# Performance work log

Hardware: AMD Instinct MI355X
Metric: run time of the kernel (lower is better)

The kernel has to match this reference:

```python
import jax, jax.numpy as jnp
import numpy as np

N = 10000      # nodes
E = 160000     # edges
F_IN = 128     # input_feature
G = 64         # graphs in batch
NC = 10        # num_classes
H1, H2, H3 = 1000, 700, 200


def _xavier(k, fi, fo):
    lim = float(np.sqrt(6.0 / (fi + fo)))
    return jax.random.uniform(k, (fi, fo), jnp.float32, -lim, lim)


def setup_inputs() -> dict:
    key = jax.random.key(0)
    ks = jax.random.split(key, 8)
    x = jax.random.normal(ks[0], (N, F_IN), jnp.float32)
    edge_index = jax.random.randint(ks[1], (2, E), 0, N)
    batch = jnp.sort(jax.random.randint(ks[2], (N,), 0, G))
    return {
        "x": x,
        "edge_index": edge_index,
        "batch": batch,
        "W1": _xavier(ks[3], F_IN, H1), "b1": jnp.zeros((H1,), jnp.float32),
        "W2": _xavier(ks[4], H1, H2),   "b2": jnp.zeros((H2,), jnp.float32),
        "W3": _xavier(ks[5], H2, H3),   "b3": jnp.zeros((H3,), jnp.float32),
        "Wl": _xavier(ks[6], H3, NC),   "bl": jnp.zeros((NC,), jnp.float32),
    }


def _gcn_conv(x, W, b, src, dst, dinv):
    # GCNConv: h = xW; out_i = sum_{j->i} d_j^-1/2 d_i^-1/2 h_j + d_i^-1 h_i + b
    h = x @ W
    coef = dinv[src] * dinv[dst]                      # [E]
    agg = jax.ops.segment_sum(h[src] * coef[:, None], dst, num_segments=N)
    agg = agg + h * (dinv * dinv)[:, None]            # self-loop term
    return agg + b


def reference(x, edge_index, batch, W1, b1, W2, b2, W3, b3, Wl, bl):
    src, dst = edge_index[0], edge_index[1]
    # degree with self-loops (edge weight 1), computed on target nodes
    deg = jax.ops.segment_sum(jnp.ones((E,), x.dtype), dst, num_segments=N) + 1.0
    dinv = jax.lax.rsqrt(deg)

    h = jax.nn.relu(_gcn_conv(x, W1, b1, src, dst, dinv))
    h = jax.nn.relu(_gcn_conv(h, W2, b2, src, dst, dinv))
    h = jax.nn.relu(_gcn_conv(h, W3, b3, src, dst, dinv))

    # global_mean_pool over graph ids
    s = jax.ops.segment_sum(h, batch, num_segments=G)
    cnt = jax.ops.segment_sum(jnp.ones((N,), h.dtype), batch, num_segments=G)
    pooled = s / jnp.maximum(cnt, 1.0)[:, None]

    # dropout is identity in eval mode
    return pooled @ Wl + bl
```

## Files before the change

### kernel.cpp

```cpp
#include <hip/hip_runtime.h>
#include <hip/hip_bf16.h>
#include <stdint.h>


#define SLOT 64

__device__ __forceinline__ uint16_t f2b(float f) {
    union { float f; uint32_t u; } v; v.f = f;
    return (uint16_t)((v.u + 0x7fffu + ((v.u >> 16) & 1u)) >> 16);
}
__device__ __forceinline__ float blo(uint32_t u) { union { uint32_t u; float f; } v; v.u = u << 16; return v.f; }
__device__ __forceinline__ float bhi(uint32_t u) { union { uint32_t u; float f; } v; v.u = u & 0xffff0000u; return v.f; }

__global__ __launch_bounds__(256) void k_scatter(
    const int* __restrict__ src, const int* __restrict__ dst,
    int* __restrict__ cursor, int* __restrict__ slots, int E, int N) {
    int g  = blockIdx.x & 7;
    int nb = gridDim.x >> 3;
    int b  = blockIdx.x >> 3;
    int seg = (N + 7) >> 3;
    int lo = g * seg;
    int hi = lo + seg; if (hi > N) hi = N;
    int per = (E + nb - 1) / nb;
    int e0 = b * per;
    int e1 = e0 + per; if (e1 > E) e1 = E;
    for (int e = e0 + threadIdx.x; e < e1; e += 256) {
        int d = dst[e];
        if (d >= lo && d < hi) {
            int s = src[e];
            int pos = atomicAdd(&cursor[d], 1);
            if (pos < SLOT) slots[d * SLOT + pos] = s;
        }
    }
}

__global__ void k_prep(const float* __restrict__ W1, const float* __restrict__ W2,
                       const float* __restrict__ W3,
                       uint16_t* __restrict__ T1, uint16_t* __restrict__ T2,
                       uint16_t* __restrict__ T3,
                       const float* __restrict__ b1, const float* __restrict__ b2,
                       const float* __restrict__ b3,
                       float* __restrict__ p1, float* __restrict__ p2,
                       float* __restrict__ p3,
                       const float* __restrict__ x, uint16_t* __restrict__ xb,
                       const int* __restrict__ deg, float* __restrict__ dinv,
                       int N, int F, int H1, int H2, int H3,
                       int Fp, int H1p, int H2p, int H3p, int n8) {
    __shared__ float tile[32][33];
    int z = blockIdx.z;
    if (z < 3) {
        const float* W; uint16_t* T; int K, Nn, Kp, Np;
        if (z == 0)      { W = W1; T = T1; K = F;  Nn = H1; Kp = Fp;  Np = H1p; }
        else if (z == 1) { W = W2; T = T2; K = H1; Nn = H2; Kp = H1p; Np = H2p; }
        else             { W = W3; T = T3; K = H2; Nn = H3; Kp = H2p; Np = H3p; }
        if ((int)blockIdx.x * 32 >= Kp || (int)blockIdx.y * 32 >= Np) return;
        int k0 = blockIdx.x * 32, n0 = blockIdx.y * 32;
        int tx = threadIdx.x, ty = threadIdx.y;
        for (int i = ty; i < 32; i += 8) {
            int k = k0 + i, n = n0 + tx;
            tile[i][tx] = (k < K && n < Nn) ? W[(size_t)k * Nn + n] : 0.f;
        }
        __syncthreads();
        for (int i = ty; i < 32; i += 8) {
            int n = n0 + i, k = k0 + tx;
            T[(size_t)n * Kp + k] = f2b(tile[tx][i]);
        }
    } else {
        int id = (blockIdx.y * gridDim.x + blockIdx.x) * 256 + threadIdx.y * 32 + threadIdx.x;
        if (z == 3) {
            if (id < H1p) p1[id] = (id < H1) ? b1[id] : 0.f;
            else if (id < H1p + H2p) { int k = id - H1p; p2[k] = (k < H2) ? b2[k] : 0.f; }
            else if (id < H1p + H2p + H3p) { int k = id - H1p - H2p; p3[k] = (k < H3) ? b3[k] : 0.f; }
        } else if (z == 4) {
            if (id < n8) {
                int node = id / (F >> 3);
                float dv = rsqrtf((float)deg[node] + 1.0f);
                const float4* x4 = (const float4*)x;
                float4 a = x4[2 * id], b = x4[2 * id + 1];
                uint4 o;
                o.x = (uint32_t)f2b(a.x * dv) | ((uint32_t)f2b(a.y * dv) << 16);
                o.y = (uint32_t)f2b(a.z * dv) | ((uint32_t)f2b(a.w * dv) << 16);
                o.z = (uint32_t)f2b(b.x * dv) | ((uint32_t)f2b(b.y * dv) << 16);
                o.w = (uint32_t)f2b(b.z * dv) | ((uint32_t)f2b(b.w * dv) << 16);
                ((uint4*)xb)[id] = o;
            }
        } else {
            if (id < N) dinv[id] = rsqrtf((float)deg[id] + 1.0f);
        }
    }
}

__global__ __launch_bounds__(256) void k_agg_panel(
    const uint16_t* __restrict__ in, uint16_t* __restrict__ out,
    const int* __restrict__ deg_, const int* __restrict__ slots,
    const float* __restrict__ dinv, const float* __restrict__ bias,
    int N, int Hc, int pc, int P, int relu) {
    int slotg = blockIdx.x & 7;
    int panel = slotg % P;
    int seg   = slotg / P;
    int nseg  = 8 / P;
    int segLen = (N + nseg - 1) / nseg;
    int wave = threadIdx.x >> 6, lane = threadIdx.x & 63;
    int half = lane >> 5, sub = lane & 31;
    int item = (blockIdx.x >> 3) * 128 + wave * 32 + sub;
    int rel = item / pc;
    if (rel >= segLen) return;
    int node = seg * segLen + rel;
    if (node >= N) return;
    int j = panel * pc + (item - rel * pc);
    int deg = deg_[node];
    if (deg > SLOT) deg = SLOT;
    int base = node * SLOT;
    float dv = dinv[node];
    const uint4* in4 = (const uint4*)in;
    float a[8] = {0.f, 0.f, 0.f, 0.f, 0.f, 0.f, 0.f, 0.f};
    if (half == 0) {
        uint4 v = in4[(size_t)node * Hc + j];
        a[0] = blo(v.x); a[1] = bhi(v.x);
        a[2] = blo(v.y); a[3] = bhi(v.y);
        a[4] = blo(v.z); a[5] = bhi(v.z);
        a[6] = blo(v.w); a[7] = bhi(v.w);
    }
    int D8 = deg & ~7;
    int e = 4 * half;
    if (e < D8) {
        int4 q = *(const int4*)&slots[base + e];
        uint4 h0 = in4[(size_t)q.x * Hc + j];
        uint4 h1 = in4[(size_t)q.y * Hc + j];
        uint4 h2 = in4[(size_t)q.z * Hc + j];
        uint4 h3 = in4[(size_t)q.w * Hc + j];
        for (e += 8; e < D8; e += 8) {
            int4 qn = *(const int4*)&slots[base + e];
            uint4 g0 = in4[(size_t)qn.x * Hc + j];
            uint4 g1 = in4[(size_t)qn.y * Hc + j];
            uint4 g2 = in4[(size_t)qn.z * Hc + j];
            uint4 g3 = in4[(size_t)qn.w * Hc + j];
            a[0] += blo(h0.x); a[1] += bhi(h0.x);
            a[2] += blo(h0.y); a[3] += bhi(h0.y);
            a[4] += blo(h0.z); a[5] += bhi(h0.z);
            a[6] += blo(h0.w); a[7] += bhi(h0.w);
            a[0] += blo(h1.x); a[1] += bhi(h1.x);
            a[2] += blo(h1.y); a[3] += bhi(h1.y);
            a[4] += blo(h1.z); a[5] += bhi(h1.z);
            a[6] += blo(h1.w); a[7] += bhi(h1.w);
            a[0] += blo(h2.x); a[1] += bhi(h2.x);
            a[2] += blo(h2.y); a[3] += bhi(h2.y);
            a[4] += blo(h2.z); a[5] += bhi(h2.z);
            a[6] += blo(h2.w); a[7] += bhi(h2.w);
            a[0] += blo(h3.x); a[1] += bhi(h3.x);
            a[2] += blo(h3.y); a[3] += bhi(h3.y);
            a[4] += blo(h3.z); a[5] += bhi(h3.z);
            a[6] += blo(h3.w); a[7] += bhi(h3.w);
            h0 = g0; h1 = g1; h2 = g2; h3 = g3;
        }
        a[0] += blo(h0.x); a[1] += bhi(h0.x);
        a[2] += blo(h0.y); a[3] += bhi(h0.y);
        a[4] += blo(h0.z); a[5] += bhi(h0.z);
        a[6] += blo(h0.w); a[7] += bhi(h0.w);
        a[0] += blo(h1.x); a[1] += bhi(h1.x);
        a[2] += blo(h1.y); a[3] += bhi(h1.y);
        a[4] += blo(h1.z); a[5] += bhi(h1.z);
        a[6] += blo(h1.w); a[7] += bhi(h1.w);
        a[0] += blo(h2.x); a[1] += bhi(h2.x);
        a[2] += blo(h2.y); a[3] += bhi(h2.y);
        a[4] += blo(h2.z); a[5] += bhi(h2.z);
        a[6] += blo(h2.w); a[7] += bhi(h2.w);
        a[0] += blo(h3.x); a[1] += bhi(h3.x);
        a[2] += blo(h3.y); a[3] += bhi(h3.y);
        a[4] += blo(h3.z); a[5] += bhi(h3.z);
        a[6] += blo(h3.w); a[7] += bhi(h3.w);
    }
    int t0 = half ? (D8 + 4 < deg ? D8 + 4 : deg) : D8;
    int t1 = half ? deg : (D8 + 4 < deg ? D8 + 4 : deg);
    for (int ee = t0; ee < t1; ++ee) {
        int s0 = slots[base + ee];
        uint4 h = in4[(size_t)s0 * Hc + j];
        a[0] += blo(h.x); a[1] += bhi(h.x);
        a[2] += blo(h.y); a[3] += bhi(h.y);
        a[4] += blo(h.z); a[5] += bhi(h.z);
        a[6] += blo(h.w); a[7] += bhi(h.w);
    }
#pragma unroll
    for (int t = 0; t < 8; ++t) a[t] += __shfl_xor(a[t], 32, 64);
    if (half == 0) {
        if (bias) {
            const float4* b4 = (const float4*)bias;
            float4 b0 = b4[2 * j], b1 = b4[2 * j + 1];
            a[0] = fmaf(a[0], dv, b0.x); a[1] = fmaf(a[1], dv, b0.y);
            a[2] = fmaf(a[2], dv, b0.z); a[3] = fmaf(a[3], dv, b0.w);
            a[4] = fmaf(a[4], dv, b1.x); a[5] = fmaf(a[5], dv, b1.y);
            a[6] = fmaf(a[6], dv, b1.z); a[7] = fmaf(a[7], dv, b1.w);
        } else {
#pragma unroll
            for (int t = 0; t < 8; ++t) a[t] *= dv;
        }
        if (relu) {
#pragma unroll
            for (int t = 0; t < 8; ++t) a[t] = fmaxf(a[t], 0.f);
        }
        uint4 o;
        o.x = (uint32_t)f2b(a[0]) | ((uint32_t)f2b(a[1]) << 16);
        o.y = (uint32_t)f2b(a[2]) | ((uint32_t)f2b(a[3]) << 16);
        o.z = (uint32_t)f2b(a[4]) | ((uint32_t)f2b(a[5]) << 16);
        o.w = (uint32_t)f2b(a[6]) | ((uint32_t)f2b(a[7]) << 16);
        ((uint4*)out)[(size_t)node * Hc + j] = o;
    }
}

__global__ __launch_bounds__(256) void k_pool_cls(
    const uint16_t* __restrict__ h, const int* __restrict__ batch,
    const float* __restrict__ Wl, const float* __restrict__ bl,
    float* __restrict__ out, int N, int H, int Hc, int NC) {
    __shared__ float part[8][26][8];
    __shared__ float pooled[200];
    int g = blockIdx.x;
    int tid = threadIdx.x;
    int lo = 0, hi = N;
    while (lo < hi) { int m = (lo + hi) >> 1; if (batch[m] < g) lo = m + 1; else hi = m; }
    int start = lo; hi = N;
    while (lo < hi) { int m = (lo + hi) >> 1; if (batch[m] < g + 1) lo = m + 1; else hi = m; }
    int end = lo;
    int j = tid & 31, s = tid >> 5;
    int jmax = H >> 3;
    const uint4* h4 = (const uint4*)h;
    if (j < jmax) {
        float a[8] = {0.f, 0.f, 0.f, 0.f, 0.f, 0.f, 0.f, 0.f};
        for (int node = start + s; node < end; node += 8) {
            uint4 v = h4[(size_t)node * Hc + j];
            a[0] += blo(v.x); a[1] += bhi(v.x);
            a[2] += blo(v.y); a[3] += bhi(v.y);
            a[4] += blo(v.z); a[5] += bhi(v.z);
            a[6] += blo(v.w); a[7] += bhi(v.w);
        }
#pragma unroll
        for (int t = 0; t < 8; ++t) part[s][j][t] = a[t];
    }
    __syncthreads();
    if (tid < H) {
        float sum = 0.f;
#pragma unroll
        for (int ss = 0; ss < 8; ++ss) sum += part[ss][tid >> 3][tid & 7];
        pooled[tid] = sum;
    }
    __syncthreads();
    if (tid < 64) {
        float scale = 1.0f / fmaxf((float)(end - start), 1.0f);
        int c = tid & 15, q = tid >> 4;
        float acc = 0.f;
        if (c < NC) {
            for (int k = q; k < H; k += 4)
                acc += pooled[k] * Wl[(size_t)k * NC + c];
        }
        acc += __shfl_xor(acc, 16, 64);
        acc += __shfl_xor(acc, 32, 64);
        if (q == 0 && c < NC) out[(size_t)g * NC + c] = acc * scale + bl[c];
    }
}

typedef __attribute__((ext_vector_type(8))) short short8;
typedef __attribute__((ext_vector_type(4))) float floatx4;

#define LDSP(p) ((__attribute__((address_space(3))) void*)(uintptr_t)(p))
#define GLBP(p) ((const __attribute__((address_space(1))) void*)(uintptr_t)(p))

__global__ __launch_bounds__(256) void k_gemm128(
    const uint16_t* __restrict__ A, const uint16_t* __restrict__ Bt,
    const float* __restrict__ bias, uint16_t* __restrict__ Cout,
    int M, int Kp, int Np, int relu, int nrg, int nr,
    const float* __restrict__ rowscale) {
    int bid = blockIdx.x;
    int rsub = bid & 7;
    int t_ = bid >> 3;
    int rg = t_ % nrg, cc = t_ / nrg;
    int rt = rg * 8 + rsub;
    if (rt >= nr) return;
    int row0 = rt * 128, col0 = cc * 128;

    __shared__ uint16_t As[128 * 64];
    __shared__ uint16_t Bs[128 * 64];
    int tid = threadIdx.x;
    int wave = tid >> 6, lane = tid & 63;
    int quad = lane >> 4, m16 = lane & 15;
    int wr = wave >> 1, wc = wave & 1;

    int rA = tid >> 3;
    int cA = (tid & 7) ^ (rA & 7);
    const uint16_t* gA = A  + (size_t)(row0 + rA) * Kp + cA * 8;
    const uint16_t* gB = Bt + (size_t)(col0 + rA) * Kp + cA * 8;
    uint16_t* lA = As + tid * 8;
    uint16_t* lB = Bs + tid * 8;
    size_t rowStep32 = (size_t)32 * Kp;

    floatx4 acc[4][4];
#pragma unroll
    for (int i = 0; i < 4; ++i)
#pragma unroll
        for (int j = 0; j < 4; ++j) acc[i][j] = (floatx4){0.f, 0.f, 0.f, 0.f};

    const short* Ash = (const short*)As;
    const short* Bsh = (const short*)Bs;
    int swA = m16 & 7;

    for (int k0 = 0; k0 < Kp; k0 += 64) {
#pragma unroll
        for (int p = 0; p < 4; ++p) {
            __builtin_amdgcn_global_load_lds(GLBP(gA + p * rowStep32), LDSP(lA + p * 2048), 16, 0, 0);
            __builtin_amdgcn_global_load_lds(GLBP(gB + p * rowStep32), LDSP(lB + p * 2048), 16, 0, 0);
        }
        gA += 64; gB += 64;
        __syncthreads();
#pragma unroll
        for (int h = 0; h < 2; ++h) {
            short8 af[4], bf[4];
            int c = h * 4 + quad;
            int pos = (c ^ swA) * 8;
#pragma unroll
            for (int i = 0; i < 4; ++i)
                af[i] = *(const short8*)&Ash[(wr * 64 + i * 16 + m16) * 64 + pos];
#pragma unroll
            for (int j = 0; j < 4; ++j)
                bf[j] = *(const short8*)&Bsh[(wc * 64 + j * 16 + m16) * 64 + pos];
#pragma unroll
            for (int i = 0; i < 4; ++i)
#pragma unroll
                for (int j = 0; j < 4; ++j)
                    acc[i][j] = __builtin_amdgcn_mfma_f32_16x16x32_bf16(af[i], bf[j], acc[i][j], 0, 0, 0);
        }
        __syncthreads();
    }

    float bv[4];
#pragma unroll
    for (int j = 0; j < 4; ++j) {
        int n = col0 + wc * 64 + j * 16 + m16;
        bv[j] = bias ? bias[n] : 0.f;
    }
#pragma unroll
    for (int i = 0; i < 4; ++i) {
        int mBase = row0 + wr * 64 + i * 16 + quad * 4;
#pragma unroll
        for (int r = 0; r < 4; ++r) {
            int m = mBase + r;
            if (m < M) {
                float s = rowscale ? rowscale[m] : 1.f;
#pragma unroll
                for (int j = 0; j < 4; ++j) {
                    int n = col0 + wc * 64 + j * 16 + m16;
                    float v = acc[i][j][r] * s + bv[j];
                    if (relu) v = fmaxf(v, 0.f);
                    Cout[(size_t)m * Np + n] = f2b(v);
                }
            }
        }
    }
}

__global__ __launch_bounds__(256) void k_gemm64(
    const uint16_t* __restrict__ A, const uint16_t* __restrict__ Bt,
    const float* __restrict__ bias, uint16_t* __restrict__ Cout,
    int M, int Kp, int Np, int relu, int nrg, int nr,
    const float* __restrict__ rowscale) {
    int bid = blockIdx.x;
    int rsub = bid & 7;
    int t_ = bid >> 3;
    int rg = t_ % nrg, cc = t_ / nrg;
    int rt = rg * 8 + rsub;
    if (rt >= nr) return;
    int row0 = rt * 128, col0 = cc * 64;

    __shared__ uint16_t As[128 * 64];
    __shared__ uint16_t Bs[64 * 64];
    int tid = threadIdx.x;
    int wave = tid >> 6, lane = tid & 63;
    int quad = lane >> 4, m16 = lane & 15;
    int wr = wave >> 1, wc = wave & 1;

    int rA = tid >> 3;
    int cA = (tid & 7) ^ (rA & 7);
    const uint16_t* gA = A  + (size_t)(row0 + rA) * Kp + cA * 8;
    const uint16_t* gB = Bt + (size_t)(col0 + rA) * Kp + cA * 8;
    uint16_t* lA = As + tid * 8;
    uint16_t* lB = Bs + tid * 8;
    size_t rowStep32 = (size_t)32 * Kp;

    floatx4 acc[4][2];
#pragma unroll
    for (int i = 0; i < 4; ++i)
#pragma unroll
        for (int j = 0; j < 2; ++j) acc[i][j] = (floatx4){0.f, 0.f, 0.f, 0.f};

    const short* Ash = (const short*)As;
    const short* Bsh = (const short*)Bs;
    int swA = m16 & 7;

    for (int k0 = 0; k0 < Kp; k0 += 64) {
#pragma unroll
        for (int p = 0; p < 4; ++p)
            __builtin_amdgcn_global_load_lds(GLBP(gA + p * rowStep32), LDSP(lA + p * 2048), 16, 0, 0);
#pragma unroll
        for (int p = 0; p < 2; ++p)
            __builtin_amdgcn_global_load_lds(GLBP(gB + p * rowStep32), LDSP(lB + p * 2048), 16, 0, 0);
        gA += 64; gB += 64;
        __syncthreads();
#pragma unroll
        for (int h = 0; h < 2; ++h) {
            short8 af[4], bf[2];
            int c = h * 4 + quad;
            int pos = (c ^ swA) * 8;
#pragma unroll
            for (int i = 0; i < 4; ++i)
                af[i] = *(const short8*)&Ash[(wr * 64 + i * 16 + m16) * 64 + pos];
#pragma unroll
            for (int j = 0; j < 2; ++j)
                bf[j] = *(const short8*)&Bsh[(wc * 32 + j * 16 + m16) * 64 + pos];
#pragma unroll
            for (int i = 0; i < 4; ++i)
#pragma unroll
                for (int j = 0; j < 2; ++j)
                    acc[i][j] = __builtin_amdgcn_mfma_f32_16x16x32_bf16(af[i], bf[j], acc[i][j], 0, 0, 0);
        }
        __syncthreads();
    }

    float bv[2];
#pragma unroll
    for (int j = 0; j < 2; ++j) {
        int n = col0 + wc * 32 + j * 16 + m16;
        bv[j] = bias ? bias[n] : 0.f;
    }
#pragma unroll
    for (int i = 0; i < 4; ++i) {
        int mBase = row0 + wr * 64 + i * 16 + quad * 4;
#pragma unroll
        for (int r = 0; r < 4; ++r) {
            int m = mBase + r;
            if (m < M) {
                float s = rowscale ? rowscale[m] : 1.f;
#pragma unroll
                for (int j = 0; j < 2; ++j) {
                    int n = col0 + wc * 32 + j * 16 + m16;
                    float v = acc[i][j][r] * s + bv[j];
                    if (relu) v = fmaxf(v, 0.f);
                    Cout[(size_t)m * Np + n] = f2b(v);
                }
            }
        }
    }
}

static inline size_t align256(size_t x) { return (x + 255) & ~(size_t)255; }
static inline int pad128(int x) { return (x + 127) & ~127; }

extern "C" void kernel_launch(void* const* d_in, const int* in_sizes, int n_in,
                              void* d_out, int out_size, void* d_ws, size_t ws_size,
                              hipStream_t stream) {
    const float* x   = (const float*)d_in[0];
    const int*   ei  = (const int*)d_in[1];
    const int*   bat = (const int*)d_in[2];
    const float* W1  = (const float*)d_in[3];
    const float* b1  = (const float*)d_in[4];
    const float* W2  = (const float*)d_in[5];
    const float* b2  = (const float*)d_in[6];
    const float* W3  = (const float*)d_in[7];
    const float* b3  = (const float*)d_in[8];
    const float* Wl  = (const float*)d_in[9];
    const float* bl  = (const float*)d_in[10];

    const int N  = in_sizes[2];
    const int E  = in_sizes[1] / 2;
    const int F  = in_sizes[0] / N;
    const int H1 = in_sizes[4];
    const int H2 = in_sizes[6];
    const int H3 = in_sizes[8];
    const int NC = in_sizes[10];
    const int G  = out_size / NC;
    const int* src = ei;
    const int* dst = ei + E;

    const int Mp  = pad128(N);
    const int Fp  = F;
    const int H1p = pad128(H1);
    const int H2p = pad128(H2);
    const int H3p = pad128(H3);

    char* p = (char*)d_ws;
    size_t off = 0;
    auto carve = [&](size_t bytes) { void* q = p + off; off += align256(bytes); return q; };
    uint16_t* xb     = (uint16_t*)carve((size_t)Mp * Fp * 2);
    uint16_t* bufA   = (uint16_t*)carve((size_t)Mp * 2048);
    uint16_t* bufB   = (uint16_t*)carve((size_t)Mp * 2048);
    uint16_t* W1t    = (uint16_t*)carve((size_t)H1p * Fp * 2);
    uint16_t* W2t    = (uint16_t*)carve((size_t)H2p * H1p * 2);
    uint16_t* W3t    = (uint16_t*)carve((size_t)H3p * H2p * 2);
    float* b1p       = (float*)carve((size_t)H1p * 4);
    float* b2p       = (float*)carve((size_t)H2p * 4);
    float* b3p       = (float*)carve((size_t)H3p * 4);
    float* dinv      = (float*)carve((size_t)N * 4);
    int*   cursor    = (int*)carve((size_t)N * 4);
    int*   slots     = (int*)carve((size_t)N * SLOT * 4);
    (void)ws_size;

    hipMemsetAsync(cursor, 0, (size_t)N * 4, stream);

    k_scatter<<<8 * 160, 256, 0, stream>>>(src, dst, cursor, slots, E, N);

    k_prep<<<dim3(32, 32, 6), dim3(32, 8), 0, stream>>>(
        W1, W2, W3, W1t, W2t, W3t, b1, b2, b3, b1p, b2p, b3p, x, xb,
        cursor, dinv, N, F, H1, H2, H3, Fp, H1p, H2p, H3p, N * F / 8);

    auto agg_grid = [&](int P, int pc) {
        int nseg = 8 / P;
        int segLen = (N + nseg - 1) / nseg;
        return 8 * ((segLen * pc + 127) / 128);
    };

    const int nr  = Mp / 128;
    const int nrg = (nr + 7) / 8;

    k_agg_panel<<<agg_grid(1, 16), 256, 0, stream>>>(
        xb, bufA, cursor, slots, dinv, nullptr, N, 16, 16, 1, 0);
    k_gemm128<<<nrg * 8 * (H1p / 128), 256, 0, stream>>>(
        bufA, W1t, b1p, bufB, N, Fp, H1p, 1, nrg, nr, nullptr);

    k_gemm128<<<nrg * 8 * (H2p / 128), 256, 0, stream>>>(
        bufB, W2t, nullptr, bufA, N, H1p, H2p, 0, nrg, nr, dinv);
    k_agg_panel<<<agg_grid(8, 11), 256, 0, stream>>>(
        bufA, bufB, cursor, slots, dinv, b2p, N, 96, 11, 8, 1);

    k_gemm64<<<nrg * 8 * (H3p / 64), 256, 0, stream>>>(
        bufB, W3t, nullptr, bufA, N, H2p, H3p, 0, nrg, nr, dinv);
    k_agg_panel<<<agg_grid(4, 7), 256, 0, stream>>>(
        bufA, bufB, cursor, slots, dinv, b3p, N, 32, 7, 4, 1);

    k_pool_cls<<<G, 256, 0, stream>>>(
        (const uint16_t*)bufB, bat, Wl, bl, (float*)d_out, N, H3, H3p >> 3, NC);
}
```

Baseline: 228.9 us.

## Fuse edge scatter into weight-prep kernel and split pooling across four blocks per graph

The edge-bucketing scatter now runs inside the weight transpose/prep kernel as an extra z-slice (1024 blocks), so weight conversion and scatter overlap in one launch. The x-to-bf16 scaling and dinv computation, which need the finished degree counts, move to a separate small kernel. Mean pooling now uses four blocks per graph that atomically accumulate partial logits into a zeroed output, raising parallelism in the tail kernel. This adds a memset and an extra launch, and makes the output summation order nondeterministic.

```diff
diff --git a/kernel.cpp b/kernel.cpp
--- a/kernel.cpp
+++ b/kernel.cpp
@@ -11,28 +11,6 @@
 }
 __device__ __forceinline__ float blo(uint32_t u) { union { uint32_t u; float f; } v; v.u = u << 16; return v.f; }
 __device__ __forceinline__ float bhi(uint32_t u) { union { uint32_t u; float f; } v; v.u = u & 0xffff0000u; return v.f; }
-
-__global__ __launch_bounds__(256) void k_scatter(
-    const int* __restrict__ src, const int* __restrict__ dst,
-    int* __restrict__ cursor, int* __restrict__ slots, int E, int N) {
-    int g  = blockIdx.x & 7;
-    int nb = gridDim.x >> 3;
-    int b  = blockIdx.x >> 3;
-    int seg = (N + 7) >> 3;
-    int lo = g * seg;
-    int hi = lo + seg; if (hi > N) hi = N;
-    int per = (E + nb - 1) / nb;
-    int e0 = b * per;
-    int e1 = e0 + per; if (e1 > E) e1 = E;
-    for (int e = e0 + threadIdx.x; e < e1; e += 256) {
-        int d = dst[e];
-        if (d >= lo && d < hi) {
-            int s = src[e];
-            int pos = atomicAdd(&cursor[d], 1);
-            if (pos < SLOT) slots[d * SLOT + pos] = s;
-        }
-    }
-}
 
 __global__ void k_prep(const float* __restrict__ W1, const float* __restrict__ W2,
                        const float* __restrict__ W3,
@@ -42,10 +20,10 @@
                        const float* __restrict__ b3,
                        float* __restrict__ p1, float* __restrict__ p2,
                        float* __restrict__ p3,
-                       const float* __restrict__ x, uint16_t* __restrict__ xb,
-                       const int* __restrict__ deg, float* __restrict__ dinv,
-                       int N, int F, int H1, int H2, int H3,
-                       int Fp, int H1p, int H2p, int H3p, int n8) {
+                       const int* __restrict__ src, const int* __restrict__ dst,
+                       int* __restrict__ cursor, int* __restrict__ slots,
+                       int E, int N, int F, int H1, int H2, int H3,
+                       int Fp, int H1p, int H2p, int H3p) {
     __shared__ float tile[32][33];
     int z = blockIdx.z;
     if (z < 3) {
@@ -65,29 +43,50 @@
             int n = n0 + i, k = k0 + tx;
             T[(size_t)n * Kp + k] = f2b(tile[tx][i]);
         }
+    } else if (z == 3) {
+        int id = (blockIdx.y * gridDim.x + blockIdx.x) * 256 + threadIdx.y * 32 + threadIdx.x;
+        if (id < H1p) p1[id] = (id < H1) ? b1[id] : 0.f;
+        else if (id < H1p + H2p) { int k = id - H1p; p2[k] = (k < H2) ? b2[k] : 0.f; }
+        else if (id < H1p + H2p + H3p) { int k = id - H1p - H2p; p3[k] = (k < H3) ? b3[k] : 0.f; }
     } else {
-        int id = (blockIdx.y * gridDim.x + blockIdx.x) * 256 + threadIdx.y * 32 + threadIdx.x;
-        if (z == 3) {
-            if (id < H1p) p1[id] = (id < H1) ? b1[id] : 0.f;
-            else if (id < H1p + H2p) { int k = id - H1p; p2[k] = (k < H2) ? b2[k] : 0.f; }
-            else if (id < H1p + H2p + H3p) { int k = id - H1p - H2p; p3[k] = (k < H3) ? b3[k] : 0.f; }
-        } else if (z == 4) {
-            if (id < n8) {
-                int node = id / (F >> 3);
-                float dv = rsqrtf((float)deg[node] + 1.0f);
-                const float4* x4 = (const float4*)x;
-                float4 a = x4[2 * id], b = x4[2 * id + 1];
-                uint4 o;
-                o.x = (uint32_t)f2b(a.x * dv) | ((uint32_t)f2b(a.y * dv) << 16);
-                o.y = (uint32_t)f2b(a.z * dv) | ((uint32_t)f2b(a.w * dv) << 16);
-                o.z = (uint32_t)f2b(b.x * dv) | ((uint32_t)f2b(b.y * dv) << 16);
-                o.w = (uint32_t)f2b(b.z * dv) | ((uint32_t)f2b(b.w * dv) << 16);
-                ((uint4*)xb)[id] = o;
+        int fb = blockIdx.y * gridDim.x + blockIdx.x;
+        int g = fb & 7, b = fb >> 3;
+        int seg = (N + 7) >> 3;
+        int lo = g * seg;
+        int hi = lo + seg; if (hi > N) hi = N;
+        int per = (E + 127) >> 7;
+        int e0 = b * per;
+        int e1 = e0 + per; if (e1 > E) e1 = E;
+        int tid = threadIdx.y * 32 + threadIdx.x;
+        for (int e = e0 + tid; e < e1; e += 256) {
+            int d = dst[e];
+            if (d >= lo && d < hi) {
+                int s = src[e];
+                int pos = atomicAdd(&cursor[d], 1);
+                if (pos < SLOT) slots[d * SLOT + pos] = s;
             }
-        } else {
-            if (id < N) dinv[id] = rsqrtf((float)deg[id] + 1.0f);
-        }
-    }
+        }
+    }
+}
+
+__global__ __launch_bounds__(256) void k_xb(
+    const float* __restrict__ x, uint16_t* __restrict__ xb,
+    const int* __restrict__ deg, float* __restrict__ dinv,
+    int N, int F, int n8) {
+    int id = blockIdx.x * 256 + threadIdx.x;
+    if (id < n8) {
+        int node = id / (F >> 3);
+        float dv = rsqrtf((float)deg[node] + 1.0f);
+        const float4* x4 = (const float4*)x;
+        float4 a = x4[2 * id], b = x4[2 * id + 1];
+        uint4 o;
+        o.x = (uint32_t)f2b(a.x * dv) | ((uint32_t)f2b(a.y * dv) << 16);
+        o.y = (uint32_t)f2b(a.z * dv) | ((uint32_t)f2b(a.w * dv) << 16);
+        o.z = (uint32_t)f2b(b.x * dv) | ((uint32_t)f2b(b.y * dv) << 16);
+        o.w = (uint32_t)f2b(b.z * dv) | ((uint32_t)f2b(b.w * dv) << 16);
+        ((uint4*)xb)[id] = o;
+    }
+    if (id < N) dinv[id] = rsqrtf((float)deg[id] + 1.0f);
 }
 
 __global__ __launch_bounds__(256) void k_agg_panel(
@@ -207,13 +206,13 @@
     }
 }
 
-__global__ __launch_bounds__(256) void k_pool_cls(
+__global__ __launch_bounds__(256) void k_pool_cls4(
     const uint16_t* __restrict__ h, const int* __restrict__ batch,
     const float* __restrict__ Wl, const float* __restrict__ bl,
     float* __restrict__ out, int N, int H, int Hc, int NC) {
     __shared__ float part[8][26][8];
     __shared__ float pooled[200];
-    int g = blockIdx.x;
+    int g = blockIdx.x >> 2, b = blockIdx.x & 3;
     int tid = threadIdx.x;
     int lo = 0, hi = N;
     while (lo < hi) { int m = (lo + hi) >> 1; if (batch[m] < g) lo = m + 1; else hi = m; }
@@ -225,7 +224,7 @@
     const uint4* h4 = (const uint4*)h;
     if (j < jmax) {
         float a[8] = {0.f, 0.f, 0.f, 0.f, 0.f, 0.f, 0.f, 0.f};
-        for (int node = start + s; node < end; node += 8) {
+        for (int node = start + s * 4 + b; node < end; node += 32) {
             uint4 v = h4[(size_t)node * Hc + j];
             a[0] += blo(v.x); a[1] += bhi(v.x);
             a[2] += blo(v.y); a[3] += bhi(v.y);
@@ -253,7 +252,11 @@
         }
         acc += __shfl_xor(acc, 16, 64);
         acc += __shfl_xor(acc, 32, 64);
-        if (q == 0 && c < NC) out[(size_t)g * NC + c] = acc * scale + bl[c];
+        if (q == 0 && c < NC) {
+            float v = acc * scale;
+            if (b == 0) v += bl[c];
+            atomicAdd(&out[(size_t)g * NC + c], v);
+        }
     }
 }
 
@@ -501,12 +504,15 @@
     (void)ws_size;
 
     hipMemsetAsync(cursor, 0, (size_t)N * 4, stream);
-
-    k_scatter<<<8 * 160, 256, 0, stream>>>(src, dst, cursor, slots, E, N);
-
-    k_prep<<<dim3(32, 32, 6), dim3(32, 8), 0, stream>>>(
-        W1, W2, W3, W1t, W2t, W3t, b1, b2, b3, b1p, b2p, b3p, x, xb,
-        cursor, dinv, N, F, H1, H2, H3, Fp, H1p, H2p, H3p, N * F / 8);
+    hipMemsetAsync(d_out, 0, (size_t)out_size * 4, stream);
+
+    k_prep<<<dim3(32, 32, 5), dim3(32, 8), 0, stream>>>(
+        W1, W2, W3, W1t, W2t, W3t, b1, b2, b3, b1p, b2p, b3p,
+        src, dst, cursor, slots,
+        E, N, F, H1, H2, H3, Fp, H1p, H2p, H3p);
+
+    k_xb<<<(N * F / 8 + 255) / 256, 256, 0, stream>>>(
+        x, xb, cursor, dinv, N, F, N * F / 8);
 
     auto agg_grid = [&](int P, int pc) {
         int nseg = 8 / P;
@@ -532,6 +538,6 @@
     k_agg_panel<<<agg_grid(4, 7), 256, 0, stream>>>(
         bufA, bufB, cursor, slots, dinv, b3p, N, 32, 7, 4, 1);
 
-    k_pool_cls<<<G, 256, 0, stream>>>(
+    k_pool_cls4<<<G * 4, 256, 0, stream>>>(
         (const uint16_t*)bufB, bat, Wl, bl, (float*)d_out, N, H3, H3p >> 3, NC);
 }
```

Result: no change. 229.3 us (+0.2%).
